# Kernel optimization log

Measured on AMD Instinct MI355X. Metric: run time of the kernel, lower is better.

The kernel has to match this reference:

```python
import jax, jax.numpy as jnp
import numpy as np

B, L, C = 4, 4096, 512
G = 4            # n_groups
H = 16           # n_heads
K = 5            # offset conv kernel == offset_range_factor
GC = C // G      # n_group_channels = 128
HC = C // H      # n_head_channels = 32


def conv1d(x, w, b, pad):
    # x: [N, Cin, L], w: [Cout, Cin, K]
    out = jax.lax.conv_general_dilated(
        x, w, window_strides=(1,), padding=[(pad, pad)],
        dimension_numbers=('NCH', 'OIH', 'NCH'))
    return out + b[None, :, None]


def grid_sample_1d(feats, gy):
    # feats: [Bg, d, L]  gy: [Bg, N] normalized coords in [-1, 1]
    # bilinear, zeros padding, align_corners=False (matches F.grid_sample)
    Bg, d, Lf = feats.shape
    N = gy.shape[-1]
    iy = ((gy + 1.0) * Lf - 1.0) * 0.5
    i0 = jnp.floor(iy)
    w1 = iy - i0
    i0 = i0.astype(jnp.int32)

    def gather(idx):
        valid = ((idx >= 0) & (idx < Lf)).astype(feats.dtype)
        idxc = jnp.clip(idx, 0, Lf - 1)
        g = jnp.take_along_axis(
            feats, jnp.broadcast_to(idxc[:, None, :], (Bg, d, N)), axis=2)
        return g * valid[:, None, :]

    return gather(i0) * (1.0 - w1)[:, None, :] + gather(i0 + 1) * w1[:, None, :]


def setup_inputs() -> dict:
    key = jax.random.key(0)
    ks = jax.random.split(key, 16)
    s = 0.02
    return {
        'x':     jax.random.normal(ks[0], (B, L, C), jnp.float32),
        'Wq':    jax.random.normal(ks[1], (C, C), jnp.float32) * s,
        'bq':    jnp.zeros((C,), jnp.float32),
        'Wk':    jax.random.normal(ks[2], (C, C), jnp.float32) * s,
        'bk':    jnp.zeros((C,), jnp.float32),
        'Wv':    jax.random.normal(ks[3], (C, C), jnp.float32) * s,
        'bv':    jnp.zeros((C,), jnp.float32),
        'Woff1': jax.random.normal(ks[4], (GC, GC, K), jnp.float32) * s,
        'boff1': jnp.zeros((GC,), jnp.float32),
        'Woff2': jax.random.normal(ks[5], (1, GC, 1), jnp.float32) * s,
        'boff2': jnp.zeros((1,), jnp.float32),
        'rpb':   jax.random.normal(ks[6], (1, C, L), jnp.float32) * s,
        'Wout':  jax.random.normal(ks[7], (C, C), jnp.float32) * s,
        'bout':  jnp.zeros((C,), jnp.float32),
    }


def reference(x, Wq, bq, Wk, bk, Wv, bv, Woff1, boff1, Woff2, boff2, rpb, Wout, bout):
    Bx, Lx, Cx = x.shape
    xc = x.transpose(0, 2, 1)                                # [B, C, L]
    # 1x1 conv projections == channel matmuls
    q = jnp.einsum('oc,bcl->bol', Wq, xc) + bq[None, :, None]
    # group queries: 'b (g d) n -> (b g) d n'
    qg = q.reshape(Bx * G, GC, Lx)
    # offset prediction: conv(k=5,pad=2) then conv(k=1,pad=2) -> length L+4
    off = conv1d(qg, Woff1, boff1, pad=K // 2)               # [Bg, GC, L]
    off = conv1d(off, Woff2, boff2, pad=K // 2)[:, 0, :]     # [Bg, L+4]
    off = jnp.tanh(off) * float(K)                           # offset_range_factor
    N = off.shape[-1]
    vgrid = jnp.arange(N, dtype=x.dtype) + off               # [Bg, L+4]
    gy = 2.0 * vgrid / float(max(N - 1, 1)) - 1.0
    # bilinear gather of grouped x, then crop to L
    xg = xc.reshape(Bx * G, GC, Lx)
    xs = grid_sample_1d(xg, gy)[:, :, :Lx]                   # [Bg, GC, L]
    xs = xs.reshape(Bx, Cx, Lx)                              # '(b g) d n -> b (g d) n'
    k = jnp.einsum('oc,bcl->bol', Wk, xs) + bk[None, :, None]
    v = jnp.einsum('oc,bcl->bol', Wv, xs) + bv[None, :, None] + rpb
    # heads: [B*H, HC, L]; attention over the CHANNEL dim (i,j = head channels)
    qh = q.reshape(Bx * H, HC, Lx)
    kh = k.reshape(Bx * H, HC, Lx)
    vh = v.reshape(Bx * H, HC, Lx)
    logits = jnp.einsum('bil,bjl->bij', qh, kh) * (Cx ** -0.5)  # [BH, HC, HC]
    attn = jax.nn.softmax(logits, axis=-1)
    o = jnp.einsum('bij,bjl->bil', attn, vh)                 # [BH, HC, L]
    # '(b g) l c -> b c (g l)' with g=H, l=HC, c=L  ->  [B, L, C]
    o = o.reshape(Bx, H, HC, Lx).transpose(0, 3, 1, 2).reshape(Bx, Lx, Cx)
    return o @ Wout.T + bout
```

## Files before the change

### kernel.cpp

```cpp
#include <hip/hip_runtime.h>
#include <math.h>

#define BB   4
#define LL   4096
#define CC   512
#define GG   4
#define HH   16
#define KW   5
#define GCC  128
#define HCC  32
#define BGN  (BB*GG)
#define BHN  (BB*HH)
#define KSPLIT 16

typedef __attribute__((ext_vector_type(8))) __bf16 bf16x8;
typedef __attribute__((ext_vector_type(4))) float f32x4;

__device__ __forceinline__ unsigned int f2bf_bits(float f) {
    unsigned int u = __float_as_uint(f);
    return (u + 0x7FFFu + ((u >> 16) & 1u)) >> 16;
}
__device__ __forceinline__ float bfbits2f(unsigned int s) {
    return __uint_as_float(s << 16);
}
__device__ __forceinline__ void split2(float v, unsigned short& h, unsigned short& l) {
    unsigned int hb = f2bf_bits(v);
    float hf = bfbits2f(hb);
    unsigned int lb = f2bf_bits(v - hf);
    h = (unsigned short)hb; l = (unsigned short)lb;
}

__device__ __forceinline__ void gload16(const void* g, void* l) {
    __builtin_amdgcn_global_load_lds(
        (const __attribute__((address_space(1))) void*)g,
        (__attribute__((address_space(3))) void*)l, 16, 0, 0);
}

__global__ __launch_bounds__(256) void split_x_kernel(
    const float* __restrict__ in, unsigned short* __restrict__ hi,
    unsigned short* __restrict__ lo, int n4)
{
    int i = blockIdx.x * 256 + threadIdx.x;
    if (i >= n4) return;
    float4 v = ((const float4*)in)[i];
    ushort4 h, l;
    split2(v.x, h.x, l.x); split2(v.y, h.y, l.y);
    split2(v.z, h.z, l.z); split2(v.w, h.w, l.w);
    ((ushort4*)hi)[i] = h;
    ((ushort4*)lo)[i] = l;
}

__global__ __launch_bounds__(256) void split_w_kernel(
    const float* __restrict__ W0, const float* __restrict__ W1,
    const float* __restrict__ W2, const float* __restrict__ W3,
    unsigned short* __restrict__ hi, unsigned short* __restrict__ lo)
{
    int w = blockIdx.y;
    const float* W = (w == 0) ? W0 : (w == 1) ? W1 : (w == 2) ? W2 : W3;
    size_t seg4 = (size_t)w * 65536;
    int i = blockIdx.x * 256 + threadIdx.x;
    float4 v = ((const float4*)W)[i];
    ushort4 h, l;
    split2(v.x, h.x, l.x); split2(v.y, h.y, l.y);
    split2(v.z, h.z, l.z); split2(v.w, h.w, l.w);
    ((ushort4*)hi)[seg4 + i] = h;
    ((ushort4*)lo)[seg4 + i] = l;
}

__global__ __launch_bounds__(256) void gemm_split_mfma(
    const unsigned short* __restrict__ Ahi, const unsigned short* __restrict__ Alo,
    const unsigned short* __restrict__ Bhi, const unsigned short* __restrict__ Blo,
    const float* __restrict__ bias, const float* __restrict__ rpb,
    float* __restrict__ out, int RA, int RB, int Kd,
    size_t aStride, size_t bStride, int biasOnCol)
{
    __shared__ unsigned short sAh[4096];
    __shared__ unsigned short sAl[4096];
    __shared__ unsigned short sBh[4096];
    __shared__ unsigned short sBl[4096];

    const int b  = blockIdx.z;
    const int c0 = blockIdx.x * 128;
    const int r0 = blockIdx.y * 128;

    const int tid  = threadIdx.x;
    const int lane = tid & 63;
    const int wv   = tid >> 6;
    const int wr   = wv >> 1, wc = wv & 1;

    const size_t laneA = (size_t)(r0 + wv * 32 + (lane >> 2)) * Kd + (size_t)((lane & 3) * 8);
    const size_t laneB = (size_t)(c0 + wv * 32 + (lane >> 2)) * Kd + (size_t)((lane & 3) * 8);
    const unsigned short* gAh = Ahi + (size_t)b * aStride + laneA;
    const unsigned short* gAl = Alo + (size_t)b * aStride + laneA;
    const unsigned short* gBh = Bhi + (size_t)b * bStride + laneB;
    const unsigned short* gBl = Blo + (size_t)b * bStride + laneB;
    const size_t rowskip = (size_t)16 * Kd;

    unsigned short* lAh = &sAh[(wv * 32) * 32];
    unsigned short* lAl = &sAl[(wv * 32) * 32];
    unsigned short* lBh = &sBh[(wv * 32) * 32];
    unsigned short* lBl = &sBl[(wv * 32) * 32];

    const int lr = lane & 15, lk = (lane >> 4) * 8;
    const unsigned short* fAh = &sAh[(wr * 64 + lr) * 32 + lk];
    const unsigned short* fAl = &sAl[(wr * 64 + lr) * 32 + lk];
    const unsigned short* fBh = &sBh[(wc * 64 + lr) * 32 + lk];
    const unsigned short* fBl = &sBl[(wc * 64 + lr) * 32 + lk];

    f32x4 acc[4][4];
#pragma unroll
    for (int i = 0; i < 4; ++i)
#pragma unroll
        for (int j = 0; j < 4; ++j) acc[i][j] = (f32x4){0.f, 0.f, 0.f, 0.f};

    for (int k0 = 0; k0 < Kd; k0 += 32) {
        gload16(gAh + k0,           lAh);
        gload16(gAh + k0 + rowskip, lAh + 512);
        gload16(gAl + k0,           lAl);
        gload16(gAl + k0 + rowskip, lAl + 512);
        gload16(gBh + k0,           lBh);
        gload16(gBh + k0 + rowskip, lBh + 512);
        gload16(gBl + k0,           lBl);
        gload16(gBl + k0 + rowskip, lBl + 512);
        __syncthreads();

        bf16x8 ah[4], al[4], bh[4], bl[4];
#pragma unroll
        for (int i = 0; i < 4; ++i) {
            ah[i] = *(const bf16x8*)(fAh + i * 512);
            al[i] = *(const bf16x8*)(fAl + i * 512);
        }
#pragma unroll
        for (int j = 0; j < 4; ++j) {
            bh[j] = *(const bf16x8*)(fBh + j * 512);
            bl[j] = *(const bf16x8*)(fBl + j * 512);
        }
#pragma unroll
        for (int i = 0; i < 4; ++i)
#pragma unroll
            for (int j = 0; j < 4; ++j) {
                acc[i][j] = __builtin_amdgcn_mfma_f32_16x16x32_bf16(ah[i], bh[j], acc[i][j], 0, 0, 0);
                acc[i][j] = __builtin_amdgcn_mfma_f32_16x16x32_bf16(al[i], bh[j], acc[i][j], 0, 0, 0);
                acc[i][j] = __builtin_amdgcn_mfma_f32_16x16x32_bf16(ah[i], bl[j], acc[i][j], 0, 0, 0);
            }
        __syncthreads();
    }

    const int lg4 = (lane >> 4) * 4;
    float bcol[4];
#pragma unroll
    for (int fj = 0; fj < 4; ++fj)
        bcol[fj] = biasOnCol ? bias[c0 + wc * 64 + fj * 16 + lr] : 0.f;

#pragma unroll
    for (int fi = 0; fi < 4; ++fi) {
#pragma unroll
        for (int reg = 0; reg < 4; ++reg) {
            const int r = r0 + wr * 64 + fi * 16 + lg4 + reg;
            const float br = biasOnCol ? 0.f : bias[r];
            float* orow = out + ((size_t)b * RA + r) * RB + c0;
            const float* prow = rpb ? (rpb + (size_t)r * RB + c0) : nullptr;
#pragma unroll
            for (int fj = 0; fj < 4; ++fj) {
                const int c = wc * 64 + fj * 16 + lr;
                float val = acc[fi][fj][reg] + br + bcol[fj];
                if (prow) val += prow[c];
                orow[c] = val;
            }
        }
    }
}

__global__ void comb_weights(const float* __restrict__ Woff1, const float* __restrict__ boff1,
                             const float* __restrict__ Woff2, const float* __restrict__ boff2,
                             float* __restrict__ wc)
{
    int idx = blockIdx.x * 256 + threadIdx.x;
    if (idx < GCC * KW) {
        int cp = idx / KW, t = idx - cp * KW;
        float s = 0.f;
        for (int c = 0; c < GCC; ++c)
            s = fmaf(Woff2[c], Woff1[((size_t)c * GCC + cp) * KW + t], s);
        wc[idx] = s;
    } else if (idx == GCC * KW) {
        float s = boff2[0];
        for (int c = 0; c < GCC; ++c) s = fmaf(Woff2[c], boff1[c], s);
        wc[idx] = s;
    } else if (idx == GCC * KW + 1) {
        wc[idx] = boff2[0];
    }
}

#define OLT 128
__global__ __launch_bounds__(128) void offsets_part_kernel(
    const float* __restrict__ q, const float* __restrict__ wc,
    float* __restrict__ part)
{
    __shared__ float sq[32][140];
    __shared__ float sw[32 * KW];

    const int l0 = blockIdx.x * OLT;
    const int bg = blockIdx.y;
    const int cg = blockIdx.z;
    const int tid = threadIdx.x;

    const float* qb = q + ((size_t)bg * GCC + cg * 32) * LL;

    for (int i = tid; i < 32 * KW; i += 128) sw[i] = wc[cg * 32 * KW + i];

    {
        const int row = tid >> 2;
        const int l4  = tid & 3;
        const float* qrow = qb + (size_t)row * LL + l0 - 8;
        for (int j = l4; j < 34; j += 4) {
            int idx = j * 4;
            float4 v;
            if (l0 - 8 + idx >= 0) v = *(const float4*)(qrow + idx);
            else v = make_float4(0.f, 0.f, 0.f, 0.f);
            *(float4*)&sq[row][idx] = v;
        }
    }
    __syncthreads();

    const int li = tid;
    float acc = 0.f;
#pragma unroll
    for (int cp = 0; cp < 32; ++cp) {
        const float* r  = &sq[cp][li + 4];
        const float* wr = &sw[cp * KW];
        acc = fmaf(wr[0], r[0], acc);
        acc = fmaf(wr[1], r[1], acc);
        acc = fmaf(wr[2], r[2], acc);
        acc = fmaf(wr[3], r[3], acc);
        acc = fmaf(wr[4], r[4], acc);
    }
    part[((size_t)cg * BGN + bg) * LL + l0 + li] = acc;
}

__global__ __launch_bounds__(256) void offsets_finish_kernel(
    const float* __restrict__ part, const float* __restrict__ wc,
    float* __restrict__ offv)
{
    int i = blockIdx.x * 256 + threadIdx.x;
    int bg = i >> 12;
    int l  = i & (LL - 1);
    float acc;
    if (l < 2) {
        acc = wc[GCC * KW + 1];
    } else {
        acc = wc[GCC * KW]
            + part[((size_t)0 * BGN + bg) * LL + l]
            + part[((size_t)1 * BGN + bg) * LL + l]
            + part[((size_t)2 * BGN + bg) * LL + l]
            + part[((size_t)3 * BGN + bg) * LL + l];
    }
    float off = tanhf(acc) * (float)KW;
    float vg  = (float)l + off;
    float iy  = vg * ((float)LL / (float)(LL + 2 * (KW / 2) - 1)) - 0.5f;
    offv[(size_t)bg * LL + l] = iy;
}

__global__ __launch_bounds__(256) void gather_kernel(
    const float* __restrict__ x, const float* __restrict__ offv,
    unsigned short* __restrict__ xshi, unsigned short* __restrict__ xslo)
{
    int bg = blockIdx.y;
    int b = bg >> 2, g = bg & 3;
    int l  = blockIdx.x * 8 + (threadIdx.x >> 5);
    int d4 = (threadIdx.x & 31) * 4;

    float iy = offv[(size_t)bg * LL + l];
    float fi = floorf(iy);
    float w1 = iy - fi;
    int i0 = (int)fi;
    int i1 = i0 + 1;

    const float* xb = x + (size_t)b * LL * CC + (size_t)g * GCC + d4;
    float4 v0 = make_float4(0.f, 0.f, 0.f, 0.f);
    float4 v1 = make_float4(0.f, 0.f, 0.f, 0.f);
    if (i0 >= 0 && i0 < LL) v0 = *(const float4*)(xb + (size_t)i0 * CC);
    if (i1 >= 0 && i1 < LL) v1 = *(const float4*)(xb + (size_t)i1 * CC);
    float w0 = 1.f - w1;
    float4 r = make_float4(v0.x * w0 + v1.x * w1, v0.y * w0 + v1.y * w1,
                           v0.z * w0 + v1.z * w1, v0.w * w0 + v1.w * w1);
    size_t o = ((size_t)b * LL + l) * CC + (size_t)g * GCC + d4;
    ushort4 h, lo4;
    split2(r.x, h.x, lo4.x); split2(r.y, h.y, lo4.y);
    split2(r.z, h.z, lo4.z); split2(r.w, h.w, lo4.w);
    *(ushort4*)(xshi + o) = h;
    *(ushort4*)(xslo + o) = lo4;
}

__global__ __launch_bounds__(64) void qk_logits(
    const float* __restrict__ q, const float* __restrict__ k,
    float* __restrict__ part)
{
    int ks = blockIdx.x, bh = blockIdx.y;
    int b = bh >> 4, h = bh & 15;
    int lane = threadIdx.x;
    int ti = lane >> 3, tj = lane & 7;
    const float* qb = q + ((size_t)b * CC + h * HCC + ti * 4) * LL;
    const float* kb = k + ((size_t)b * CC + h * HCC + tj * 4) * LL;

    float acc[4][4];
#pragma unroll
    for (int i = 0; i < 4; ++i)
#pragma unroll
        for (int j = 0; j < 4; ++j) acc[i][j] = 0.f;

    const int chunk = LL / KSPLIT;
    int l0 = ks * chunk;
    for (int l = l0; l < l0 + chunk; l += 8) {
        float4 qa[4][2], kv[4][2];
#pragma unroll
        for (int p = 0; p < 4; ++p) {
            qa[p][0] = *(const float4*)(qb + (size_t)p * LL + l);
            qa[p][1] = *(const float4*)(qb + (size_t)p * LL + l + 4);
            kv[p][0] = *(const float4*)(kb + (size_t)p * LL + l);
            kv[p][1] = *(const float4*)(kb + (size_t)p * LL + l + 4);
        }
#pragma unroll
        for (int i = 0; i < 4; ++i)
#pragma unroll
            for (int j = 0; j < 4; ++j) {
                float s = acc[i][j];
                s = fmaf(qa[i][0].x, kv[j][0].x, s);
                s = fmaf(qa[i][0].y, kv[j][0].y, s);
                s = fmaf(qa[i][0].z, kv[j][0].z, s);
                s = fmaf(qa[i][0].w, kv[j][0].w, s);
                s = fmaf(qa[i][1].x, kv[j][1].x, s);
                s = fmaf(qa[i][1].y, kv[j][1].y, s);
                s = fmaf(qa[i][1].z, kv[j][1].z, s);
                s = fmaf(qa[i][1].w, kv[j][1].w, s);
                acc[i][j] = s;
            }
    }
#pragma unroll
    for (int i = 0; i < 4; ++i)
#pragma unroll
        for (int j = 0; j < 4; ++j)
            part[(((size_t)bh * KSPLIT + ks) * HCC + ti * 4 + i) * HCC + tj * 4 + j] = acc[i][j];
}

__global__ __launch_bounds__(64) void softmax_kernel(
    const float* __restrict__ part, float* __restrict__ attn)
{
    int bh = blockIdx.x;
    int i = threadIdx.x;
    if (i >= HCC) return;
    const float SCALE = 0.044194173824159216f;

    float lg[HCC];
    float mx = -1e30f;
#pragma unroll
    for (int j = 0; j < HCC; ++j) {
        float s = 0.f;
        for (int ks = 0; ks < KSPLIT; ++ks)
            s += part[(((size_t)bh * KSPLIT + ks) * HCC + i) * HCC + j];
        s *= SCALE;
        lg[j] = s;
        mx = fmaxf(mx, s);
    }
    float sum = 0.f;
#pragma unroll
    for (int j = 0; j < HCC; ++j) {
        float e = expf(lg[j] - mx);
        lg[j] = e;
        sum += e;
    }
    float inv = 1.f / sum;
#pragma unroll
    for (int j = 0; j < HCC; ++j)
        attn[((size_t)bh * HCC + i) * HCC + j] = lg[j] * inv;
}

__global__ __launch_bounds__(256) void attn_v_kernel(
    const float* __restrict__ attn, const float* __restrict__ v,
    unsigned short* __restrict__ ohi, unsigned short* __restrict__ olo)
{
    int bh = blockIdx.y;
    int b = bh >> 4, h = bh & 15;
    int tid = threadIdx.x;
    int i = tid >> 3, lsub = tid & 7;

    float arow[HCC];
#pragma unroll
    for (int j = 0; j < HCC; ++j)
        arow[j] = attn[((size_t)bh * HCC + i) * HCC + j];

    const float* vb = v + ((size_t)b * CC + h * HCC) * LL;
    __shared__ float os[HCC][65];

    for (int l0 = blockIdx.x * 512; l0 < blockIdx.x * 512 + 512; l0 += 64) {
        int lbase = l0 + lsub * 8;
        float4 a0 = make_float4(0.f, 0.f, 0.f, 0.f);
        float4 a1 = make_float4(0.f, 0.f, 0.f, 0.f);
#pragma unroll 8
        for (int j = 0; j < HCC; ++j) {
            float aw = arow[j];
            float4 v0 = *(const float4*)(vb + (size_t)j * LL + lbase);
            float4 v1 = *(const float4*)(vb + (size_t)j * LL + lbase + 4);
            a0.x = fmaf(aw, v0.x, a0.x); a0.y = fmaf(aw, v0.y, a0.y);
            a0.z = fmaf(aw, v0.z, a0.z); a0.w = fmaf(aw, v0.w, a0.w);
            a1.x = fmaf(aw, v1.x, a1.x); a1.y = fmaf(aw, v1.y, a1.y);
            a1.z = fmaf(aw, v1.z, a1.z); a1.w = fmaf(aw, v1.w, a1.w);
        }
        os[i][lsub*8+0] = a0.x; os[i][lsub*8+1] = a0.y;
        os[i][lsub*8+2] = a0.z; os[i][lsub*8+3] = a0.w;
        os[i][lsub*8+4] = a1.x; os[i][lsub*8+5] = a1.y;
        os[i][lsub*8+6] = a1.z; os[i][lsub*8+7] = a1.w;
        __syncthreads();
        int i2 = tid & 31, lw = tid >> 5;
#pragma unroll
        for (int c = 0; c < 8; ++c) {
            int ll = lw * 8 + c;
            float val = os[i2][ll];
            unsigned short hbits, lbits;
            split2(val, hbits, lbits);
            size_t oidx = ((size_t)b * LL + l0 + ll) * CC + h * HCC + i2;
            ohi[oidx] = hbits;
            olo[oidx] = lbits;
        }
        __syncthreads();
    }
}

extern "C" void kernel_launch(void* const* d_in, const int* in_sizes, int n_in,
                              void* d_out, int out_size, void* d_ws, size_t ws_size,
                              hipStream_t stream)
{
    (void)in_sizes; (void)n_in; (void)out_size; (void)ws_size;
    const float* x     = (const float*)d_in[0];
    const float* Wq    = (const float*)d_in[1];
    const float* bq    = (const float*)d_in[2];
    const float* Wk    = (const float*)d_in[3];
    const float* bk    = (const float*)d_in[4];
    const float* Wv    = (const float*)d_in[5];
    const float* bv    = (const float*)d_in[6];
    const float* Woff1 = (const float*)d_in[7];
    const float* boff1 = (const float*)d_in[8];
    const float* Woff2 = (const float*)d_in[9];
    const float* boff2 = (const float*)d_in[10];
    const float* rpb   = (const float*)d_in[11];
    const float* Wout  = (const float*)d_in[12];
    const float* bout  = (const float*)d_in[13];
    float* out = (float*)d_out;

    float* ws = (float*)d_ws;
    float* q    = ws;
    float* kbuf = ws + 8388608;
    float* vbuf = ws + 16777216;
    unsigned short* dhi = (unsigned short*)(ws + 25165824);
    unsigned short* dlo = (unsigned short*)(ws + 25165824 + 4194304);
    unsigned short* whi = (unsigned short*)(ws + 33554432);
    unsigned short* wlo = (unsigned short*)(ws + 33554432 + 524288);
    float* offv = ws + 34603008;
    float* wcmb = ws + 34668544;
    float* part = ws + 34669568;
    float* attn = ws + 35718144;

    const size_t NK = (size_t)LL * CC;

    comb_weights<<<dim3(3), dim3(256), 0, stream>>>(Woff1, boff1, Woff2, boff2, wcmb);
    split_w_kernel<<<dim3(256, 4), dim3(256), 0, stream>>>(Wq, Wk, Wv, Wout, whi, wlo);
    split_x_kernel<<<dim3(8192), dim3(256), 0, stream>>>(x, dhi, dlo, 2097152);

    gemm_split_mfma<<<dim3(32, 4, 4), dim3(256), 0, stream>>>(
        whi + 0 * 262144, wlo + 0 * 262144, dhi, dlo, bq, nullptr,
        q, CC, LL, CC, 0, NK, 0);

    offsets_part_kernel<<<dim3(32, 16, 4), dim3(128), 0, stream>>>(q, wcmb, part);
    offsets_finish_kernel<<<dim3(256), dim3(256), 0, stream>>>(part, wcmb, offv);
    gather_kernel<<<dim3(512, 16), dim3(256), 0, stream>>>(x, offv, dhi, dlo);

    gemm_split_mfma<<<dim3(32, 4, 4), dim3(256), 0, stream>>>(
        whi + 1 * 262144, wlo + 1 * 262144, dhi, dlo, bk, nullptr,
        kbuf, CC, LL, CC, 0, NK, 0);
    gemm_split_mfma<<<dim3(32, 4, 4), dim3(256), 0, stream>>>(
        whi + 2 * 262144, wlo + 2 * 262144, dhi, dlo, bv, rpb,
        vbuf, CC, LL, CC, 0, NK, 0);

    qk_logits<<<dim3(KSPLIT, BHN), dim3(64), 0, stream>>>(q, kbuf, part);
    softmax_kernel<<<dim3(BHN), dim3(64), 0, stream>>>(part, attn);
    attn_v_kernel<<<dim3(8, BHN), dim3(256), 0, stream>>>(attn, vbuf, dhi, dlo);

    gemm_split_mfma<<<dim3(4, 32, 4), dim3(256), 0, stream>>>(
        dhi, dlo, whi + 3 * 262144, wlo + 3 * 262144, bout, nullptr,
        out, LL, CC, CC, NK, 0, 1);
}
```

Before: 401.5 us.

## Double-buffer LDS tiles and XOR-swizzle layout in split-bf16 MFMA GEMM

The GEMM main loop now uses two LDS buffers, so the global-to-LDS loads for the next K tile are issued before the MFMAs on the current tile, and only one barrier per iteration remains. The LDS layout is also XOR-swizzled: the global load chunk index and the fragment read index are permuted so the bf16x8 reads hit fewer LDS bank conflicts. This doubles shared memory per block to 64 KB, which can reduce occupancy. Correctness depends on the swizzle on the write side matching the read side.

Measured after the change: 404.3 us. Within noise of the previous version (+0.7%).

```diff
diff --git a/kernel.cpp b/kernel.cpp
--- a/kernel.cpp
+++ b/kernel.cpp
@@ -74,10 +74,7 @@
     float* __restrict__ out, int RA, int RB, int Kd,
     size_t aStride, size_t bStride, int biasOnCol)
 {
-    __shared__ unsigned short sAh[4096];
-    __shared__ unsigned short sAl[4096];
-    __shared__ unsigned short sBh[4096];
-    __shared__ unsigned short sBl[4096];
+    __shared__ unsigned short sm[2][4][4096];
 
     const int b  = blockIdx.z;
     const int c0 = blockIdx.x * 128;
@@ -88,24 +85,21 @@
     const int wv   = tid >> 6;
     const int wr   = wv >> 1, wc = wv & 1;
 
-    const size_t laneA = (size_t)(r0 + wv * 32 + (lane >> 2)) * Kd + (size_t)((lane & 3) * 8);
-    const size_t laneB = (size_t)(c0 + wv * 32 + (lane >> 2)) * Kd + (size_t)((lane & 3) * 8);
+    const int srow   = lane >> 2;
+    const int schunk = (lane & 3) ^ ((lane >> 3) & 3);
+    const size_t laneA = (size_t)(r0 + wv * 32 + srow) * Kd + (size_t)(schunk * 8);
+    const size_t laneB = (size_t)(c0 + wv * 32 + srow) * Kd + (size_t)(schunk * 8);
     const unsigned short* gAh = Ahi + (size_t)b * aStride + laneA;
     const unsigned short* gAl = Alo + (size_t)b * aStride + laneA;
     const unsigned short* gBh = Bhi + (size_t)b * bStride + laneB;
     const unsigned short* gBl = Blo + (size_t)b * bStride + laneB;
     const size_t rowskip = (size_t)16 * Kd;
-
-    unsigned short* lAh = &sAh[(wv * 32) * 32];
-    unsigned short* lAl = &sAl[(wv * 32) * 32];
-    unsigned short* lBh = &sBh[(wv * 32) * 32];
-    unsigned short* lBl = &sBl[(wv * 32) * 32];
-
-    const int lr = lane & 15, lk = (lane >> 4) * 8;
-    const unsigned short* fAh = &sAh[(wr * 64 + lr) * 32 + lk];
-    const unsigned short* fAl = &sAl[(wr * 64 + lr) * 32 + lk];
-    const unsigned short* fBh = &sBh[(wc * 64 + lr) * 32 + lk];
-    const unsigned short* fBl = &sBl[(wc * 64 + lr) * 32 + lk];
+    const int ldsOff = wv * 1024;
+
+    const int lr = lane & 15;
+    const int kx = ((lane >> 4) ^ ((lane >> 1) & 3)) * 8;
+    const int aOff = (wr * 64 + lr) * 32 + kx;
+    const int bOff = (wc * 64 + lr) * 32 + kx;
 
     f32x4 acc[4][4];
 #pragma unroll
@@ -113,38 +107,67 @@
 #pragma unroll
         for (int j = 0; j < 4; ++j) acc[i][j] = (f32x4){0.f, 0.f, 0.f, 0.f};
 
-    for (int k0 = 0; k0 < Kd; k0 += 32) {
-        gload16(gAh + k0,           lAh);
-        gload16(gAh + k0 + rowskip, lAh + 512);
-        gload16(gAl + k0,           lAl);
-        gload16(gAl + k0 + rowskip, lAl + 512);
-        gload16(gBh + k0,           lBh);
-        gload16(gBh + k0 + rowskip, lBh + 512);
-        gload16(gBl + k0,           lBl);
-        gload16(gBl + k0 + rowskip, lBl + 512);
+    bf16x8 ah[4], al[4], bh[4], bl[4];
+
+#define STAGE(buf, k0)                                                        \
+    {                                                                         \
+        unsigned short* d0 = &sm[buf][0][ldsOff];                             \
+        gload16(gAh + (k0), d0);  gload16(gAh + (k0) + rowskip, d0 + 512);    \
+        unsigned short* d1 = &sm[buf][1][ldsOff];                             \
+        gload16(gAl + (k0), d1);  gload16(gAl + (k0) + rowskip, d1 + 512);    \
+        unsigned short* d2 = &sm[buf][2][ldsOff];                             \
+        gload16(gBh + (k0), d2);  gload16(gBh + (k0) + rowskip, d2 + 512);    \
+        unsigned short* d3 = &sm[buf][3][ldsOff];                             \
+        gload16(gBl + (k0), d3);  gload16(gBl + (k0) + rowskip, d3 + 512);    \
+    }
+
+#define LOADF(buf)                                                            \
+    {                                                                         \
+        const unsigned short* mAh = &sm[buf][0][aOff];                        \
+        const unsigned short* mAl = &sm[buf][1][aOff];                        \
+        const unsigned short* mBh = &sm[buf][2][bOff];                        \
+        const unsigned short* mBl = &sm[buf][3][bOff];                        \
+        _Pragma("unroll")                                                     \
+        for (int i = 0; i < 4; ++i) {                                         \
+            ah[i] = *(const bf16x8*)(mAh + i * 512);                          \
+            al[i] = *(const bf16x8*)(mAl + i * 512);                          \
+        }                                                                     \
+        _Pragma("unroll")                                                     \
+        for (int j = 0; j < 4; ++j) {                                         \
+            bh[j] = *(const bf16x8*)(mBh + j * 512);                          \
+            bl[j] = *(const bf16x8*)(mBl + j * 512);                          \
+        }                                                                     \
+    }
+
+#define DOMFMA                                                                \
+    {                                                                         \
+        _Pragma("unroll")                                                     \
+        for (int i = 0; i < 4; ++i)                                           \
+            _Pragma("unroll")                                                 \
+            for (int j = 0; j < 4; ++j) {                                     \
+                acc[i][j] = __builtin_amdgcn_mfma_f32_16x16x32_bf16(ah[i], bh[j], acc[i][j], 0, 0, 0); \
+                acc[i][j] = __builtin_amdgcn_mfma_f32_16x16x32_bf16(al[i], bh[j], acc[i][j], 0, 0, 0); \
+                acc[i][j] = __builtin_amdgcn_mfma_f32_16x16x32_bf16(ah[i], bl[j], acc[i][j], 0, 0, 0); \
+            }                                                                 \
+    }
+
+    STAGE(0, 0)
+    __syncthreads();
+
+    int cur = 0;
+    for (int k0 = 0; k0 + 32 < Kd; k0 += 32) {
+        LOADF(cur)
+        STAGE(cur ^ 1, k0 + 32)
+        DOMFMA
         __syncthreads();
-
-        bf16x8 ah[4], al[4], bh[4], bl[4];
-#pragma unroll
-        for (int i = 0; i < 4; ++i) {
-            ah[i] = *(const bf16x8*)(fAh + i * 512);
-            al[i] = *(const bf16x8*)(fAl + i * 512);
-        }
-#pragma unroll
-        for (int j = 0; j < 4; ++j) {
-            bh[j] = *(const bf16x8*)(fBh + j * 512);
-            bl[j] = *(const bf16x8*)(fBl + j * 512);
-        }
-#pragma unroll
-        for (int i = 0; i < 4; ++i)
-#pragma unroll
-            for (int j = 0; j < 4; ++j) {
-                acc[i][j] = __builtin_amdgcn_mfma_f32_16x16x32_bf16(ah[i], bh[j], acc[i][j], 0, 0, 0);
-                acc[i][j] = __builtin_amdgcn_mfma_f32_16x16x32_bf16(al[i], bh[j], acc[i][j], 0, 0, 0);
-                acc[i][j] = __builtin_amdgcn_mfma_f32_16x16x32_bf16(ah[i], bl[j], acc[i][j], 0, 0, 0);
-            }
-        __syncthreads();
-    }
+        cur ^= 1;
+    }
+    LOADF(cur)
+    DOMFMA
+
+#undef STAGE
+#undef LOADF
+#undef DOMFMA
 
     const int lg4 = (lane >> 4) * 4;
     float bcol[4];
```
